# Kernel tuning notes

Hardware: AMD Instinct MI355X
Metric: run time of the kernel (lower is better)

Reference implementation:

```python
import jax, jax.numpy as jnp
import numpy as np

LN_EPS = 1e-5

def _normalize_adj(adj):
    # D^{-1/2} A D^{-1/2} via broadcast row/col scaling (same math as diag matmuls)
    deg = jnp.clip(adj.sum(axis=1), 1e-6, None)
    d = deg ** -0.5
    return d[:, None] * adj * d[None, :]

def _layer_norm(x, g, b):
    mu = x.mean(axis=-1, keepdims=True)
    var = ((x - mu) ** 2).mean(axis=-1, keepdims=True)
    return (x - mu) * jax.lax.rsqrt(var + LN_EPS) * g + b

def setup_inputs() -> dict:
    key = jax.random.key(0)
    ks = jax.random.split(key, 8)
    N, E, H = 8192, 256, 256
    x = jax.random.normal(ks[0], (N, E), dtype=jnp.float32)
    adj = jax.random.uniform(ks[1], (N, N), dtype=jnp.float32)
    # Linear weights stored torch-style (out_dim, in_dim), xavier-uniform
    def xavier(k, out_d, in_d):
        lim = float(np.sqrt(6.0 / (in_d + out_d)))
        return jax.random.uniform(k, (out_d, in_d), minval=-lim, maxval=lim, dtype=jnp.float32)
    W1 = xavier(ks[2], H, E); b1 = jnp.zeros((H,), jnp.float32)
    W2 = xavier(ks[3], E, H); b2 = jnp.zeros((E,), jnp.float32)
    g1 = jnp.ones((H,), jnp.float32); beta1 = jnp.zeros((H,), jnp.float32)
    g2 = jnp.ones((E,), jnp.float32); beta2 = jnp.zeros((E,), jnp.float32)
    return {"x": x, "adj": adj, "W1": W1, "b1": b1, "g1": g1, "beta1": beta1,
            "W2": W2, "b2": b2, "g2": g2, "beta2": beta2}

def reference(x, adj, W1, b1, g1, beta1, W2, b2, g2, beta2):
    adj_norm = _normalize_adj(adj)  # shared across layers (same adj)
    residual = x
    # layer 1: aggregate -> linear -> LN -> GELU (dropout=eval identity)
    h = adj_norm @ x
    h = h @ W1.T + b1
    h = jax.nn.gelu(_layer_norm(h, g1, beta1), approximate=False)
    # layer 2
    h = adj_norm @ h
    h = h @ W2.T + b2
    h = jax.nn.gelu(_layer_norm(h, g2, beta2), approximate=False)
    return h + residual
```

## Files before the change

### kernel.cpp

```cpp
#include <hip/hip_runtime.h>
#include <hip/hip_bf16.h>
#include <math.h>

#define LN_EPS 1e-5f

typedef __attribute__((ext_vector_type(4))) float fx4;
typedef __attribute__((ext_vector_type(8))) short s8v;

__device__ inline unsigned f2bf(float f) {
  unsigned u = __builtin_bit_cast(unsigned, f);
  return (u + 0x7fffu + ((u >> 16) & 1u)) >> 16;
}
__device__ inline unsigned pk2(float a, float b) {
  return f2bf(a) | (f2bf(b) << 16);
}

__global__ __launch_bounds__(256) void prep_adj(const float* __restrict__ adj,
                                                float* __restrict__ dv,
                                                uint4* __restrict__ Af) {
  const int tid = threadIdx.x;
  const int m0 = blockIdx.x * 16;
  const int r = tid & 15;
  const int cg = tid >> 4;
  const float* src = adj + (long)(m0 + r) * 8192 + cg * 8;
  uint4* wbase = Af + (((long)(blockIdx.x >> 2) * 256) * 4 + (blockIdx.x & 3)) * 64 + (tid & 63);
  const int ksub = tid >> 6;

  float s = 0.f;
  #pragma unroll 4
  for (int p = 0; p < 64; ++p) {
    float4 a = *(const float4*)(src + p * 128);
    float4 b = *(const float4*)(src + p * 128 + 4);
    s += (a.x + a.y) + (a.z + a.w) + (b.x + b.y) + (b.z + b.w);
    uint4 o;
    o.x = pk2(a.x, a.y); o.y = pk2(a.z, a.w);
    o.z = pk2(b.x, b.y); o.w = pk2(b.z, b.w);
    wbase[(long)(p * 4 + ksub) * 256] = o;
  }
  s += __shfl_xor(s, 16);
  s += __shfl_xor(s, 32);
  __shared__ float red[4][16];
  if ((tid & 63) < 16) red[tid >> 6][r] = s;
  __syncthreads();
  if (tid < 16) {
    float t = (red[0][tid] + red[1][tid]) + (red[2][tid] + red[3][tid]);
    dv[m0 + tid] = rsqrtf(fmaxf(t, 1e-6f));
  }
}

__global__ __launch_bounds__(256) void build_xt(const float* __restrict__ x,
                                                const float* __restrict__ dv,
                                                unsigned short* __restrict__ xt) {
  __shared__ float t[64][257];
  const int tid = threadIdx.x;
  const int k0 = blockIdx.x * 64;
  #pragma unroll
  for (int i = 0; i < 16; ++i) {
    int idx = i * 1024 + tid * 4;
    int r = idx >> 8, c = idx & 255;
    float4 v = *(const float4*)(x + (long)(k0 + r) * 256 + c);
    float dd = dv[k0 + r];
    t[r][c] = v.x * dd; t[r][c + 1] = v.y * dd;
    t[r][c + 2] = v.z * dd; t[r][c + 3] = v.w * dd;
  }
  __syncthreads();
  const int n = tid;
  unsigned short* dst = xt + (long)blockIdx.x * 16384 + n * 64;
  #pragma unroll
  for (int gg = 0; gg < 8; ++gg) {
    int q = gg ^ (n & 7);
    uint4 o;
    #pragma unroll
    for (int jj = 0; jj < 4; ++jj) {
      int k = gg * 8 + jj * 2;
      ((unsigned*)&o)[jj] = pk2(t[k][n], t[k + 1][n]);
    }
    *(uint4*)(dst + q * 8) = o;
  }
}

__global__ __launch_bounds__(256) void cvt_w(const float* __restrict__ w,
                                             unsigned short* __restrict__ wb, int n) {
  int i = blockIdx.x * 256 + threadIdx.x;
  if (i * 4 < n) {
    float4 v = *(const float4*)(w + i * 4);
    uint2 o;
    o.x = pk2(v.x, v.y); o.y = pk2(v.z, v.w);
    *(uint2*)(wb + i * 4) = o;
  }
}

#define BM 128
#define BN 256

__global__ __launch_bounds__(512) void gemm_big(const uint4* __restrict__ Af,
                                                const unsigned short* __restrict__ Bt,
                                                float* __restrict__ Cp, int kchunk) {
  __shared__ __align__(16) unsigned short Bl[2][BN * 64];
  const int tid = threadIdx.x, lane = tid & 63, w = tid >> 6;
  const int wm = w >> 1, wn = w & 1;
  const long bx = blockIdx.x, by = blockIdx.y;
  const int kbase = (int)by * kchunk;
  const int NT = kchunk >> 6;

  const uint4* ap = Af + (((bx * 2 + (wm >> 1)) * 256 + (kbase >> 5)) * 4 + (wm & 1) * 2) * 64 + lane;
  const unsigned short* bsrc = Bt + (long)(kbase >> 6) * 16384 + w * 2048 + lane * 8;

  uint4 abA[4], abB[4];
  fx4 acc[2][8] = {};

  auto loadA = [&](int kt, uint4 (&d)[4]) {
    #pragma unroll
    for (int mf = 0; mf < 2; ++mf)
      #pragma unroll
      for (int kk = 0; kk < 2; ++kk)
        d[mf * 2 + kk] = ap[((long)kt * 8 + kk * 4 + mf) * 64];
  };
  auto stageB = [&](int kt, int buf) {
    #pragma unroll
    for (int i = 0; i < 4; ++i)
      __builtin_amdgcn_global_load_lds(
          (const unsigned int*)(bsrc + (long)kt * 16384 + i * 512),
          (unsigned int*)&Bl[buf][(w * 4 + i) * 512], 16, 0, 0);
  };
  auto compute = [&](uint4 (&ab)[4], int buf) {
    #pragma unroll
    for (int kk = 0; kk < 2; ++kk) {
      #pragma unroll
      for (int nf = 0; nf < 8; ++nf) {
        int n = wn * 128 + nf * 16 + (lane & 15);
        int k8 = kk * 4 + (lane >> 4);
        const s8v bf = *(const s8v*)&Bl[buf][n * 64 + ((k8 ^ (n & 7)) << 3)];
        #pragma unroll
        for (int mf = 0; mf < 2; ++mf)
          acc[mf][nf] = __builtin_amdgcn_mfma_f32_16x16x32_bf16(
              *(const s8v*)&ab[mf * 2 + kk], bf, acc[mf][nf], 0, 0, 0);
      }
    }
  };

  loadA(0, abA); stageB(0, 0);
  asm volatile("s_waitcnt vmcnt(0)" ::: "memory");
  __syncthreads();
  for (int kt = 0; kt < NT; kt += 2) {
    if (kt + 1 < NT) { stageB(kt + 1, 1); loadA(kt + 1, abB); }
    compute(abA, 0);
    asm volatile("s_waitcnt vmcnt(0)" ::: "memory");
    __syncthreads();
    if (kt + 2 < NT) { stageB(kt + 2, 0); loadA(kt + 2, abA); }
    if (kt + 1 < NT) {
      compute(abB, 1);
      asm volatile("s_waitcnt vmcnt(0)" ::: "memory");
      __syncthreads();
    }
  }

  float* outp = Cp + (by * 8192 + bx * BM) * 256;
  #pragma unroll
  for (int mf = 0; mf < 2; ++mf)
    #pragma unroll
    for (int nf = 0; nf < 8; ++nf)
      #pragma unroll
      for (int j = 0; j < 4; ++j) {
        int r = wm * 32 + mf * 16 + (lane >> 4) * 4 + j;
        int cc = wn * 128 + nf * 16 + (lane & 15);
        outp[(long)r * 256 + cc] = acc[mf][nf][j];
      }
}

template <int LAYER2>
__global__ __launch_bounds__(256) void epi_kernel(const float* __restrict__ Cp, int splitk,
                                                  const float* __restrict__ dv,
                                                  const unsigned short* __restrict__ Wb,
                                                  const float* __restrict__ bias,
                                                  const float* __restrict__ g,
                                                  const float* __restrict__ beta,
                                                  const float* __restrict__ xres,
                                                  unsigned short* __restrict__ xtOut,
                                                  float* __restrict__ out) {
  __shared__ __align__(16) unsigned short hA[32 * 256];
  __shared__ float Zl[32][257];
  __shared__ float redS[4][32], redSS[4][32];
  __shared__ float stats[32][2];
  const int tid = threadIdx.x, lane = tid & 63, w = tid >> 6;
  const int m0 = blockIdx.x * 32;

  #pragma unroll
  for (int i = 0; i < 8; ++i) {
    int idx = i * 1024 + tid * 4;
    int r = idx >> 8, c = idx & 255;
    float sx = 0.f, sy = 0.f, sz = 0.f, sw = 0.f;
    for (int sk = 0; sk < splitk; ++sk) {
      float4 v = *(const float4*)(Cp + ((long)sk * 8192 + m0 + r) * 256 + c);
      sx += v.x; sy += v.y; sz += v.z; sw += v.w;
    }
    float dd = dv[m0 + r];
    uint2 o;
    o.x = pk2(sx * dd, sy * dd); o.y = pk2(sz * dd, sw * dd);
    *(uint2*)&hA[r * 256 + (c ^ ((r & 7) << 3))] = o;
  }
  __syncthreads();

  fx4 acc[8] = {};
  const int row = (w >> 1) * 16 + (lane & 15);
  #pragma unroll
  for (int k0 = 0; k0 < 256; k0 += 32) {
    int kc = k0 + (lane >> 4) * 8;
    s8v a = *(const s8v*)&hA[row * 256 + (kc ^ ((row & 7) << 3))];
    #pragma unroll
    for (int nf = 0; nf < 8; ++nf) {
      int n = (w & 1) * 128 + nf * 16 + (lane & 15);
      s8v b = *(const s8v*)(Wb + (long)n * 256 + kc);
      acc[nf] = __builtin_amdgcn_mfma_f32_16x16x32_bf16(a, b, acc[nf], 0, 0, 0);
    }
  }

  #pragma unroll
  for (int nf = 0; nf < 8; ++nf)
    #pragma unroll
    for (int j = 0; j < 4; ++j) {
      int r = (w >> 1) * 16 + (lane >> 4) * 4 + j;
      int cc = (w & 1) * 128 + nf * 16 + (lane & 15);
      Zl[r][cc] = acc[nf][j] + bias[cc];
    }
  __syncthreads();

  {
    int r = tid & 31, q = tid >> 5;
    float s = 0.f, ss = 0.f;
    #pragma unroll
    for (int c = 0; c < 32; ++c) {
      float v = Zl[r][q * 32 + c];
      s += v; ss += v * v;
    }
    s += __shfl_xor(s, 32); ss += __shfl_xor(ss, 32);
    if (lane < 32) { redS[w][r] = s; redSS[w][r] = ss; }
  }
  __syncthreads();
  if (tid < 32) {
    float s = (redS[0][tid] + redS[1][tid]) + (redS[2][tid] + redS[3][tid]);
    float ss = (redSS[0][tid] + redSS[1][tid]) + (redSS[2][tid] + redSS[3][tid]);
    float mu = s * (1.f / 256.f);
    float var = ss * (1.f / 256.f) - mu * mu;
    stats[tid][0] = mu; stats[tid][1] = rsqrtf(var + LN_EPS);
  }
  __syncthreads();

  {
    int r = tid & 31, q = tid >> 5;
    float mu = stats[r][0], inv = stats[r][1];
    float dd = LAYER2 ? 1.f : dv[m0 + r];
    #pragma unroll
    for (int c = 0; c < 32; ++c) {
      int cc = q * 32 + c;
      float v = (Zl[r][cc] - mu) * inv * g[cc] + beta[cc];
      float ge = 0.5f * v * (1.f + erff(v * 0.70710678118f));
      Zl[r][cc] = ge * dd;
    }
  }
  __syncthreads();

  if (!LAYER2) {
    int n = tid;
    unsigned short* dst = xtOut + ((long)(m0 >> 6)) * 16384 + n * 64;
    int g0 = (m0 & 32) >> 3;
    #pragma unroll
    for (int gi = 0; gi < 4; ++gi) {
      int gg = g0 + gi;
      int q = gg ^ (n & 7);
      uint4 o;
      #pragma unroll
      for (int jj = 0; jj < 4; ++jj) {
        int rr = gi * 8 + jj * 2;
        ((unsigned*)&o)[jj] = pk2(Zl[rr][n], Zl[rr + 1][n]);
      }
      *(uint4*)(dst + q * 8) = o;
    }
  } else {
    int c = tid;
    #pragma unroll 8
    for (int r = 0; r < 32; ++r) {
      long idx = (long)(m0 + r) * 256 + c;
      out[idx] = Zl[r][c] + xres[idx];
    }
  }
}

extern "C" void kernel_launch(void* const* d_in, const int* in_sizes, int n_in,
                              void* d_out, int out_size, void* d_ws, size_t ws_size,
                              hipStream_t stream) {
  const float* x   = (const float*)d_in[0];
  const float* adj = (const float*)d_in[1];
  const float* W1  = (const float*)d_in[2];
  const float* b1  = (const float*)d_in[3];
  const float* g1  = (const float*)d_in[4];
  const float* be1 = (const float*)d_in[5];
  const float* W2  = (const float*)d_in[6];
  const float* b2  = (const float*)d_in[7];
  const float* g2  = (const float*)d_in[8];
  const float* be2 = (const float*)d_in[9];
  float* out = (float*)d_out;

  char* ws = (char*)d_ws;
  size_t off = 0;
  uint4* Af = (uint4*)(ws); off += 134217728;
  unsigned short* X1T = (unsigned short*)(ws + off); off += 4194304;
  unsigned short* X2T = (unsigned short*)(ws + off); off += 4194304;
  unsigned short* W1b = (unsigned short*)(ws + off); off += 131072;
  unsigned short* W2b = (unsigned short*)(ws + off); off += 131072;
  float* dvec = (float*)(ws + off); off += 32768;
  float* Cpart = (float*)(ws + off);

  int splitk = 4;
  while (splitk > 1 && off + (size_t)splitk * 8192 * 256 * 4 > ws_size) splitk >>= 1;
  int kchunk = 8192 / splitk;

  prep_adj<<<512, 256, 0, stream>>>(adj, dvec, Af);
  build_xt<<<128, 256, 0, stream>>>(x, dvec, X1T);
  cvt_w<<<64, 256, 0, stream>>>(W1, W1b, 65536);
  cvt_w<<<64, 256, 0, stream>>>(W2, W2b, 65536);

  gemm_big<<<dim3(64, splitk), 512, 0, stream>>>(Af, X1T, Cpart, kchunk);
  epi_kernel<0><<<256, 256, 0, stream>>>(Cpart, splitk, dvec, W1b, b1, g1, be1,
                                         nullptr, X2T, nullptr);
  gemm_big<<<dim3(64, splitk), 512, 0, stream>>>(Af, X2T, Cpart, kchunk);
  epi_kernel<1><<<256, 256, 0, stream>>>(Cpart, splitk, dvec, W2b, b2, g2, be2,
                                         x, nullptr, out);
}
```

Baseline: 255.5 us.

## Retile gemm waves to 64x64, store split-K partials in fp16, relax waitcnt

After: 259.1 us. Within noise of the previous version (+1.4%).

```diff
diff --git a/kernel.cpp b/kernel.cpp
--- a/kernel.cpp
+++ b/kernel.cpp
@@ -6,6 +6,7 @@
 
 typedef __attribute__((ext_vector_type(4))) float fx4;
 typedef __attribute__((ext_vector_type(8))) short s8v;
+typedef __attribute__((ext_vector_type(2))) _Float16 h2v;
 
 __device__ inline unsigned f2bf(float f) {
   unsigned u = __builtin_bit_cast(unsigned, f);
@@ -13,6 +14,9 @@
 }
 __device__ inline unsigned pk2(float a, float b) {
   return f2bf(a) | (f2bf(b) << 16);
+}
+__device__ inline unsigned short f2h(float f) {
+  return __builtin_bit_cast(unsigned short, (_Float16)f);
 }
 
 __global__ __launch_bounds__(256) void prep_adj(const float* __restrict__ adj,
@@ -95,23 +99,23 @@
 
 __global__ __launch_bounds__(512) void gemm_big(const uint4* __restrict__ Af,
                                                 const unsigned short* __restrict__ Bt,
-                                                float* __restrict__ Cp, int kchunk) {
+                                                unsigned short* __restrict__ Cp, int kchunk) {
   __shared__ __align__(16) unsigned short Bl[2][BN * 64];
   const int tid = threadIdx.x, lane = tid & 63, w = tid >> 6;
-  const int wm = w >> 1, wn = w & 1;
+  const int wm = w >> 2, wn = w & 3;
   const long bx = blockIdx.x, by = blockIdx.y;
   const int kbase = (int)by * kchunk;
   const int NT = kchunk >> 6;
 
-  const uint4* ap = Af + (((bx * 2 + (wm >> 1)) * 256 + (kbase >> 5)) * 4 + (wm & 1) * 2) * 64 + lane;
+  const uint4* ap = Af + (((bx * 2 + wm) * 256 + (kbase >> 5)) * 4) * 64 + lane;
   const unsigned short* bsrc = Bt + (long)(kbase >> 6) * 16384 + w * 2048 + lane * 8;
 
-  uint4 abA[4], abB[4];
-  fx4 acc[2][8] = {};
-
-  auto loadA = [&](int kt, uint4 (&d)[4]) {
-    #pragma unroll
-    for (int mf = 0; mf < 2; ++mf)
+  uint4 abA[8], abB[8];
+  fx4 acc[4][4] = {};
+
+  auto loadA = [&](int kt, uint4 (&d)[8]) {
+    #pragma unroll
+    for (int mf = 0; mf < 4; ++mf)
       #pragma unroll
       for (int kk = 0; kk < 2; ++kk)
         d[mf * 2 + kk] = ap[((long)kt * 8 + kk * 4 + mf) * 64];
@@ -123,53 +127,55 @@
           (const unsigned int*)(bsrc + (long)kt * 16384 + i * 512),
           (unsigned int*)&Bl[buf][(w * 4 + i) * 512], 16, 0, 0);
   };
-  auto compute = [&](uint4 (&ab)[4], int buf) {
+  auto compute = [&](uint4 (&ab)[8], int buf) {
     #pragma unroll
     for (int kk = 0; kk < 2; ++kk) {
       #pragma unroll
-      for (int nf = 0; nf < 8; ++nf) {
-        int n = wn * 128 + nf * 16 + (lane & 15);
+      for (int nf = 0; nf < 4; ++nf) {
+        int n = wn * 64 + nf * 16 + (lane & 15);
         int k8 = kk * 4 + (lane >> 4);
         const s8v bf = *(const s8v*)&Bl[buf][n * 64 + ((k8 ^ (n & 7)) << 3)];
         #pragma unroll
-        for (int mf = 0; mf < 2; ++mf)
+        for (int mf = 0; mf < 4; ++mf)
           acc[mf][nf] = __builtin_amdgcn_mfma_f32_16x16x32_bf16(
               *(const s8v*)&ab[mf * 2 + kk], bf, acc[mf][nf], 0, 0, 0);
       }
     }
   };
 
-  loadA(0, abA); stageB(0, 0);
-  asm volatile("s_waitcnt vmcnt(0)" ::: "memory");
+  stageB(0, 0); loadA(0, abA);
+  asm volatile("s_waitcnt vmcnt(8)" ::: "memory");
   __syncthreads();
   for (int kt = 0; kt < NT; kt += 2) {
-    if (kt + 1 < NT) { stageB(kt + 1, 1); loadA(kt + 1, abB); }
+    stageB(kt + 1, 1); loadA(kt + 1, abB);
     compute(abA, 0);
-    asm volatile("s_waitcnt vmcnt(0)" ::: "memory");
+    asm volatile("s_waitcnt vmcnt(8)" ::: "memory");
     __syncthreads();
-    if (kt + 2 < NT) { stageB(kt + 2, 0); loadA(kt + 2, abA); }
-    if (kt + 1 < NT) {
+    if (kt + 2 < NT) {
+      stageB(kt + 2, 0); loadA(kt + 2, abA);
       compute(abB, 1);
-      asm volatile("s_waitcnt vmcnt(0)" ::: "memory");
+      asm volatile("s_waitcnt vmcnt(8)" ::: "memory");
       __syncthreads();
-    }
-  }
-
-  float* outp = Cp + (by * 8192 + bx * BM) * 256;
-  #pragma unroll
-  for (int mf = 0; mf < 2; ++mf)
-    #pragma unroll
-    for (int nf = 0; nf < 8; ++nf)
+    } else {
+      compute(abB, 1);
+    }
+  }
+
+  unsigned short* outp = Cp + (by * 8192 + bx * BM) * 256;
+  #pragma unroll
+  for (int mf = 0; mf < 4; ++mf)
+    #pragma unroll
+    for (int nf = 0; nf < 4; ++nf)
       #pragma unroll
       for (int j = 0; j < 4; ++j) {
-        int r = wm * 32 + mf * 16 + (lane >> 4) * 4 + j;
-        int cc = wn * 128 + nf * 16 + (lane & 15);
-        outp[(long)r * 256 + cc] = acc[mf][nf][j];
+        int r = wm * 64 + mf * 16 + (lane >> 4) * 4 + j;
+        int cc = wn * 64 + nf * 16 + (lane & 15);
+        outp[(long)r * 256 + cc] = f2h(acc[mf][nf][j]);
       }
 }
 
 template <int LAYER2>
-__global__ __launch_bounds__(256) void epi_kernel(const float* __restrict__ Cp, int splitk,
+__global__ __launch_bounds__(256) void epi_kernel(const unsigned short* __restrict__ Cp, int splitk,
                                                   const float* __restrict__ dv,
                                                   const unsigned short* __restrict__ Wb,
                                                   const float* __restrict__ bias,
@@ -191,8 +197,11 @@
     int r = idx >> 8, c = idx & 255;
     float sx = 0.f, sy = 0.f, sz = 0.f, sw = 0.f;
     for (int sk = 0; sk < splitk; ++sk) {
-      float4 v = *(const float4*)(Cp + ((long)sk * 8192 + m0 + r) * 256 + c);
-      sx += v.x; sy += v.y; sz += v.z; sw += v.w;
+      uint2 v = *(const uint2*)(Cp + ((long)sk * 8192 + m0 + r) * 256 + c);
+      h2v p0 = __builtin_bit_cast(h2v, v.x);
+      h2v p1 = __builtin_bit_cast(h2v, v.y);
+      sx += (float)p0.x; sy += (float)p0.y;
+      sz += (float)p1.x; sw += (float)p1.y;
     }
     float dd = dv[m0 + r];
     uint2 o;
@@ -309,10 +318,10 @@
   unsigned short* W1b = (unsigned short*)(ws + off); off += 131072;
   unsigned short* W2b = (unsigned short*)(ws + off); off += 131072;
   float* dvec = (float*)(ws + off); off += 32768;
-  float* Cpart = (float*)(ws + off);
+  unsigned short* Cpart = (unsigned short*)(ws + off);
 
   int splitk = 4;
-  while (splitk > 1 && off + (size_t)splitk * 8192 * 256 * 4 > ws_size) splitk >>= 1;
+  while (splitk > 1 && off + (size_t)splitk * 8192 * 256 * 2 > ws_size) splitk >>= 1;
   int kchunk = 8192 / splitk;
 
   prep_adj<<<512, 256, 0, stream>>>(adj, dvec, Af);
```
